# Performance work log

Measured on AMD Instinct MI355X. Metric: run time of the kernel, lower is better.

Reference implementation:

```python
import jax, jax.numpy as jnp
import numpy as np

D_MODEL = 1024
NHEAD = 16
DFF = 4096
EPS = 1e-5


def layer_norm(x, g, b, eps=EPS):
    mu = jnp.mean(x, axis=-1, keepdims=True)
    var = jnp.var(x, axis=-1, keepdims=True)
    return (x - mu) * jax.lax.rsqrt(var + eps) * g + b


def setup_inputs() -> dict:
    key = jax.random.key(0)
    ks = jax.random.split(key, 8)
    S, N, E = 1024, 8, D_MODEL
    s = 0.02
    return {
        "src": jax.random.normal(ks[0], (S, N, E), dtype=jnp.float32),
        "in_proj_w": jax.random.normal(ks[1], (3 * E, E), dtype=jnp.float32) * s,
        "in_proj_b": jnp.zeros((3 * E,), dtype=jnp.float32),
        "out_w": jax.random.normal(ks[2], (E, E), dtype=jnp.float32) * s,
        "out_b": jnp.zeros((E,), dtype=jnp.float32),
        "w1": jax.random.normal(ks[3], (DFF, E), dtype=jnp.float32) * s,
        "b1": jnp.zeros((DFF,), dtype=jnp.float32),
        "w2": jax.random.normal(ks[4], (E, DFF), dtype=jnp.float32) * s,
        "b2": jnp.zeros((E,), dtype=jnp.float32),
        "ln1_g": jnp.ones((E,), dtype=jnp.float32),
        "ln1_b": jnp.zeros((E,), dtype=jnp.float32),
        "ln2_g": jnp.ones((E,), dtype=jnp.float32),
        "ln2_b": jnp.zeros((E,), dtype=jnp.float32),
    }


def reference(src, in_proj_w, in_proj_b, out_w, out_b, w1, b1, w2, b2,
              ln1_g, ln1_b, ln2_g, ln2_b):
    S, N, E = src.shape
    H = NHEAD
    D = E // H
    scale = 1.0 / jnp.sqrt(jnp.asarray(D, src.dtype))

    # fused QKV projection (PyTorch in_proj): [S,N,3E]
    qkv = src @ in_proj_w.T + in_proj_b
    q, k, v = jnp.split(qkv, 3, axis=-1)
    # [S,N,E] -> [N,H,S,D]
    def to_heads(t):
        return t.reshape(S, N, H, D).transpose(1, 2, 0, 3)
    q, k, v = to_heads(q), to_heads(k), to_heads(v)

    # explicit QK^T / softmax / AV (need_weights=True path)
    scores = jnp.einsum('nhsd,nhtd->nhst', q * scale, k)  # [N,H,S,S]
    attn = jax.nn.softmax(scores, axis=-1)
    ctx = jnp.einsum('nhst,nhtd->nhsd', attn, v)          # [N,H,S,D]
    ctx = ctx.transpose(2, 0, 1, 3).reshape(S, N, E)
    attn_out = ctx @ out_w.T + out_b

    # avg over heads (PyTorch default average_attn_weights=True): [N,S,S]
    attn_weights = jnp.mean(attn, axis=1)

    # post-norm residual structure (norm_first=False), dropout=0 (eval)
    x = layer_norm(src + attn_out, ln1_g, ln1_b)
    ff = jax.nn.relu(x @ w1.T + b1) @ w2.T + b2
    x = layer_norm(x + ff, ln2_g, ln2_b)
    return x, attn_weights
```

## Files before the change

kernel.cpp:

```cpp
#include <hip/hip_runtime.h>

typedef __attribute__((ext_vector_type(4))) float f32x4;
typedef __attribute__((ext_vector_type(8))) short short8;
typedef __attribute__((ext_vector_type(4))) unsigned short u16x4;

#define MFMA(a,b,c) __builtin_amdgcn_mfma_f32_16x16x32_bf16(a,b,c,0,0,0)

__device__ __forceinline__ unsigned short f2bf(float x){
    union { float f; unsigned int u; } c; c.f = x;
    unsigned int u = c.u;
    unsigned int r = (u + 0x7fffu + ((u >> 16) & 1u)) >> 16;
    return (unsigned short)r;
}
__device__ __forceinline__ float bf2f(unsigned short h){
    union { unsigned int u; float f; } c; c.u = ((unsigned int)h) << 16;
    return c.f;
}

__device__ __forceinline__ void load16_lds(const unsigned short* g, unsigned short* l){
    __builtin_amdgcn_global_load_lds(
        (const __attribute__((address_space(1))) unsigned int*)g,
        (__attribute__((address_space(3))) unsigned int*)l, 16, 0, 0);
}

#define SWZ_IDX(row, col, stride) \
    ((row)*(stride) + (((((col) >> 3) ^ ((row) & 7)) << 3) | ((col) & 7)))

__global__ __launch_bounds__(256) void cast_f32_bf16(const float* __restrict__ in,
                                                     unsigned short* __restrict__ out, int n4){
    int i = blockIdx.x * 256 + threadIdx.x;
    if (i < n4){
        const float4* in4 = (const float4*)in;
        float4 v = in4[i];
        u16x4 o;
        o[0] = f2bf(v.x); o[1] = f2bf(v.y); o[2] = f2bf(v.z); o[3] = f2bf(v.w);
        ((u16x4*)out)[i] = o;
    }
}

template<int OUT_BF16, int RELU>
__global__ __launch_bounds__(256) void gemm_bt(const unsigned short* __restrict__ A,
                                               const unsigned short* __restrict__ W,
                                               const float* __restrict__ bias,
                                               void* __restrict__ Cout,
                                               int M, int N, int K)
{
    __shared__ unsigned short As[128*32];
    __shared__ unsigned short Bs[128*32];
    const int tid  = threadIdx.x;
    const int wave = tid >> 6, lane = tid & 63;
    const int bm = blockIdx.x, bn = blockIdx.y;
    const int wr = wave >> 1, wc = wave & 1;
    const int lr = lane & 15, lg = lane >> 4;

    f32x4 acc[4][4] = {};

    const size_t arow0 = (size_t)bm * 128;
    const size_t brow0 = (size_t)bn * 128;

    for (int k0 = 0; k0 < K; k0 += 32){
        __syncthreads();
        #pragma unroll
        for (int i = 0; i < 2; ++i){
            int c = i*256 + wave*64 + lane;
            int row = c >> 2, cc = c & 3;
            load16_lds(A + (arow0 + row)*K + k0 + cc*8, As + (size_t)(i*256 + wave*64)*8);
            load16_lds(W + (brow0 + row)*K + k0 + cc*8, Bs + (size_t)(i*256 + wave*64)*8);
        }
        __syncthreads();
        short8 af[4], bfr[4];
        #pragma unroll
        for (int mi = 0; mi < 4; ++mi)
            af[mi] = *(const short8*)(As + (wr*64 + mi*16 + lr)*32 + lg*8);
        #pragma unroll
        for (int ni = 0; ni < 4; ++ni)
            bfr[ni] = *(const short8*)(Bs + (wc*64 + ni*16 + lr)*32 + lg*8);
        #pragma unroll
        for (int mi = 0; mi < 4; ++mi)
            #pragma unroll
            for (int ni = 0; ni < 4; ++ni)
                acc[mi][ni] = MFMA(af[mi], bfr[ni], acc[mi][ni]);
    }

    #pragma unroll
    for (int ni = 0; ni < 4; ++ni){
        int col = bn*128 + wc*64 + ni*16 + lr;
        float bv = bias ? bias[col] : 0.0f;
        #pragma unroll
        for (int mi = 0; mi < 4; ++mi){
            int row0 = bm*128 + wr*64 + mi*16 + lg*4;
            #pragma unroll
            for (int j = 0; j < 4; ++j){
                float v = acc[mi][ni][j] + bv;
                if (RELU) v = v > 0.0f ? v : 0.0f;
                if (OUT_BF16) ((unsigned short*)Cout)[(size_t)(row0+j)*N + col] = f2bf(v);
                else          ((float*)Cout)[(size_t)(row0+j)*N + col] = v;
            }
        }
    }
}

__global__ __launch_bounds__(256) void transpose_v(const unsigned short* __restrict__ qkv,
                                                   unsigned short* __restrict__ vt)
{
    __shared__ unsigned short tile[64][80];
    const int tt = blockIdx.x, h = blockIdx.y, n = blockIdx.z;
    const int tid = threadIdx.x;
    #pragma unroll
    for (int i = 0; i < 2; ++i){
        int c = i*256 + tid;
        int row = c >> 3, cc = c & 7;
        short8 v = *(const short8*)(qkv + ((size_t)(tt*64+row)*8 + n)*3072 + 2048 + h*64 + cc*8);
        *(short8*)&tile[row][cc*8] = v;
    }
    __syncthreads();
    #pragma unroll
    for (int i = 0; i < 2; ++i){
        int c = i*256 + tid;
        int drow = c >> 3, cc = c & 7;
        short8 o;
        #pragma unroll
        for (int j = 0; j < 8; ++j) o[j] = tile[cc*8+j][drow];
        *(short8*)(vt + ((size_t)(n*16+h)*64 + drow)*1024 + tt*64 + cc*8) = o;
    }
}

__global__ __launch_bounds__(256) void attn_fused(const unsigned short* __restrict__ qkv,
                                                  const unsigned short* __restrict__ vt,
                                                  float2* __restrict__ stats,
                                                  unsigned short* __restrict__ ctx)
{
    __shared__ unsigned short qs[32*64];
    __shared__ unsigned short kt[64*64];
    __shared__ unsigned short vtile[64*64];
    __shared__ unsigned short pt[32*64];
    __shared__ float wl[4][32];
    __shared__ float rowinv[32];
    const int qb = blockIdx.x, h = blockIdx.y, n = blockIdx.z;
    const int tid = threadIdx.x;
    const int wave = tid >> 6, lane = tid & 63;
    const int lr = lane & 15, lg = lane >> 4;
    const int s0 = qb * 32;
    const float scale = 0.125f;

    {
        int row = tid >> 3, cc = tid & 7;
        *(short8*)(qs + SWZ_IDX(row, cc*8, 64)) =
            *(const short8*)(qkv + ((size_t)(s0+row)*8 + n)*3072 + h*64 + cc*8);
    }

    float lsum[2][4] = {};
    f32x4 av[2] = {};

    for (int tt = 0; tt < 16; ++tt){
        __syncthreads();
        #pragma unroll
        for (int i = 0; i < 2; ++i){
            int c = i*256 + wave*64 + lane;
            int row = c >> 3, sl = (c & 7) ^ (row & 7);
            load16_lds(qkv + ((size_t)(tt*64+row)*8 + n)*3072 + 1024 + h*64 + sl*8,
                       kt + (size_t)(i*256 + wave*64)*8);
            load16_lds(vt + ((size_t)(n*16+h)*64 + row)*1024 + tt*64 + sl*8,
                       vtile + (size_t)(i*256 + wave*64)*8);
        }
        __syncthreads();

        f32x4 acc[2] = {};
        #pragma unroll
        for (int kk = 0; kk < 2; ++kk){
            short8 b  = *(const short8*)(kt + SWZ_IDX(wave*16 + lr, kk*32 + lg*8, 64));
            short8 a0 = *(const short8*)(qs + SWZ_IDX(lr,          kk*32 + lg*8, 64));
            short8 a1 = *(const short8*)(qs + SWZ_IDX(16 + lr,     kk*32 + lg*8, 64));
            acc[0] = MFMA(a0, b, acc[0]);
            acc[1] = MFMA(a1, b, acc[1]);
        }
        #pragma unroll
        for (int mi = 0; mi < 2; ++mi)
            #pragma unroll
            for (int j = 0; j < 4; ++j){
                float p = __expf(fminf(acc[mi][j] * scale, 80.0f));
                lsum[mi][j] += p;
                pt[SWZ_IDX(mi*16 + lg*4 + j, wave*16 + lr, 64)] = f2bf(p);
            }
        __syncthreads();

        #pragma unroll
        for (int kk = 0; kk < 2; ++kk){
            short8 b  = *(const short8*)(vtile + SWZ_IDX(wave*16 + lr, kk*32 + lg*8, 64));
            short8 a0 = *(const short8*)(pt + SWZ_IDX(lr,      kk*32 + lg*8, 64));
            short8 a1 = *(const short8*)(pt + SWZ_IDX(16 + lr, kk*32 + lg*8, 64));
            av[0] = MFMA(a0, b, av[0]);
            av[1] = MFMA(a1, b, av[1]);
        }
    }

    #pragma unroll
    for (int mi = 0; mi < 2; ++mi)
        #pragma unroll
        for (int j = 0; j < 4; ++j){
            float v = lsum[mi][j];
            v += __shfl_xor(v, 1);
            v += __shfl_xor(v, 2);
            v += __shfl_xor(v, 4);
            v += __shfl_xor(v, 8);
            if (lr == 0) wl[wave][mi*16 + lg*4 + j] = v;
        }
    __syncthreads();
    if (tid < 32){
        float l = wl[0][tid] + wl[1][tid] + wl[2][tid] + wl[3][tid];
        float inv = 1.0f / l;
        rowinv[tid] = inv;
        stats[((size_t)(n*16+h)*1024) + s0 + tid] = make_float2(0.0f, inv * 0.0625f);
    }
    __syncthreads();

    #pragma unroll
    for (int mi = 0; mi < 2; ++mi)
        #pragma unroll
        for (int j = 0; j < 4; ++j){
            int lrow = mi*16 + lg*4 + j;
            int srow = s0 + lrow;
            int d = wave*16 + lr;
            ctx[((size_t)srow*8 + n)*1024 + h*64 + d] = f2bf(av[mi][j] * rowinv[lrow]);
        }
}

__global__ __launch_bounds__(256) void attn_mean(const unsigned short* __restrict__ qkv,
                                                 const float2* __restrict__ stats,
                                                 float* __restrict__ attw)
{
    __shared__ unsigned short qs[16*256];
    __shared__ unsigned short kv[64*256];
    __shared__ float2 smL[16][16];
    const int qb = blockIdx.x, n = blockIdx.y;
    const int tid = threadIdx.x;
    const int wave = tid >> 6, lane = tid & 63;
    const int lr = lane & 15, lg = lane >> 4;
    const int s0 = qb * 16;
    const float scale = 0.125f;

    {
        int head = tid >> 4, row = tid & 15;
        smL[head][row] = stats[((size_t)(n*16+head)*1024) + s0 + row];
    }

    f32x4 racc[16];
    #pragma unroll
    for (int t = 0; t < 16; ++t) racc[t] = (f32x4){0.0f,0.0f,0.0f,0.0f};

    for (int g = 0; g < 4; ++g){
        __syncthreads();
        #pragma unroll
        for (int i = 0; i < 2; ++i){
            int c = i*256 + tid;
            int row = c >> 5, cc = c & 31;
            *(short8*)(qs + SWZ_IDX(row, cc*8, 256)) =
                *(const short8*)(qkv + ((size_t)(s0+row)*8 + n)*3072 + g*256 + cc*8);
        }
        #pragma unroll
        for (int tt = 0; tt < 16; ++tt){
            __syncthreads();
            #pragma unroll
            for (int i = 0; i < 8; ++i){
                int c = i*256 + wave*64 + lane;
                int row = c >> 5, sd = c & 31;
                int sl = sd ^ (row & 7);
                load16_lds(qkv + ((size_t)(tt*64+row)*8 + n)*3072 + 1024 + g*256 + sl*8,
                           kv + (size_t)(i*256 + wave*64)*8);
            }
            __syncthreads();
            #pragma unroll
            for (int hh = 0; hh < 4; ++hh){
                f32x4 acc = {0.0f,0.0f,0.0f,0.0f};
                #pragma unroll
                for (int kk = 0; kk < 2; ++kk){
                    short8 b = *(const short8*)(kv + SWZ_IDX(wave*16 + lr, hh*64 + kk*32 + lg*8, 256));
                    short8 a = *(const short8*)(qs + SWZ_IDX(lr,           hh*64 + kk*32 + lg*8, 256));
                    acc = MFMA(a, b, acc);
                }
                #pragma unroll
                for (int j = 0; j < 4; ++j){
                    float2 mc = smL[g*4 + hh][lg*4 + j];
                    racc[tt][j] += __expf(fminf(acc[j]*scale, 80.0f) - mc.x) * mc.y;
                }
            }
        }
    }
    float* base = attw + (size_t)n*1024*1024;
    #pragma unroll
    for (int tt = 0; tt < 16; ++tt)
        #pragma unroll
        for (int j = 0; j < 4; ++j)
            base[(size_t)(s0 + lg*4 + j)*1024 + tt*64 + wave*16 + lr] = racc[tt][j];
}

__global__ __launch_bounds__(256) void add_ln(const float* __restrict__ a,
                                              const float* __restrict__ b,
                                              const float* __restrict__ g,
                                              const float* __restrict__ be,
                                              float* __restrict__ out32,
                                              unsigned short* __restrict__ outbf)
{
    __shared__ float red[8];
    const int row = blockIdx.x;
    const int tid = threadIdx.x;
    const int wave = tid >> 6, lane = tid & 63;
    float4 va = ((const float4*)(a + (size_t)row*1024))[tid];
    float4 vb = ((const float4*)(b + (size_t)row*1024))[tid];
    float x0 = va.x + vb.x, x1 = va.y + vb.y, x2 = va.z + vb.z, x3 = va.w + vb.w;
    float s  = x0 + x1 + x2 + x3;
    float sq = x0*x0 + x1*x1 + x2*x2 + x3*x3;
    #pragma unroll
    for (int off = 1; off < 64; off <<= 1){
        s  += __shfl_xor(s,  off);
        sq += __shfl_xor(sq, off);
    }
    if (lane == 0){ red[wave] = s; red[4+wave] = sq; }
    __syncthreads();
    s  = red[0] + red[1] + red[2] + red[3];
    sq = red[4] + red[5] + red[6] + red[7];
    float mean = s * (1.0f/1024.0f);
    float var  = sq * (1.0f/1024.0f) - mean*mean;
    float rstd = rsqrtf(var + 1e-5f);
    int c = tid * 4;
    float4 vg = ((const float4*)(g  + c))[0];
    float4 vbeta = ((const float4*)(be + c))[0];
    float y0 = (x0-mean)*rstd*vg.x + vbeta.x;
    float y1 = (x1-mean)*rstd*vg.y + vbeta.y;
    float y2 = (x2-mean)*rstd*vg.z + vbeta.z;
    float y3 = (x3-mean)*rstd*vg.w + vbeta.w;
    float4 o; o.x=y0; o.y=y1; o.z=y2; o.w=y3;
    ((float4*)(out32 + (size_t)row*1024))[tid] = o;
    if (outbf){
        u16x4 ob; ob[0]=f2bf(y0); ob[1]=f2bf(y1); ob[2]=f2bf(y2); ob[3]=f2bf(y3);
        ((u16x4*)(outbf + (size_t)row*1024))[tid] = ob;
    }
}

extern "C" void kernel_launch(void* const* d_in, const int* in_sizes, int n_in,
                              void* d_out, int out_size, void* d_ws, size_t ws_size,
                              hipStream_t stream)
{
    (void)in_sizes; (void)n_in; (void)out_size; (void)ws_size;
    const float* src  = (const float*)d_in[0];
    const float* wqkv = (const float*)d_in[1];
    const float* bqkv = (const float*)d_in[2];
    const float* wout = (const float*)d_in[3];
    const float* bout = (const float*)d_in[4];
    const float* w1   = (const float*)d_in[5];
    const float* b1   = (const float*)d_in[6];
    const float* w2   = (const float*)d_in[7];
    const float* b2   = (const float*)d_in[8];
    const float* g1   = (const float*)d_in[9];
    const float* be1  = (const float*)d_in[10];
    const float* g2   = (const float*)d_in[11];
    const float* be2  = (const float*)d_in[12];

    char* ws = (char*)d_ws;
    const size_t MB = 1ull << 20;
    unsigned short* wqkv_bf = (unsigned short*)(ws + 0*MB);
    unsigned short* wout_bf = (unsigned short*)(ws + 6*MB);
    unsigned short* w1_bf   = (unsigned short*)(ws + 8*MB);
    unsigned short* w2_bf   = (unsigned short*)(ws + 16*MB);
    unsigned short* src_bf  = (unsigned short*)(ws + 24*MB);
    unsigned short* x1_bf   = (unsigned short*)(ws + 24*MB);
    unsigned short* qkv_bf  = (unsigned short*)(ws + 40*MB);
    unsigned short* vt_bf   = (unsigned short*)(ws + 88*MB);
    unsigned short* ff1_bf  = (unsigned short*)(ws + 40*MB);
    unsigned short* ctx_bf  = (unsigned short*)(ws + 104*MB);
    float* attn_out = (float*)(ws + 120*MB);
    float* ff2_f32  = (float*)(ws + 120*MB);
    float* x1_f32   = (float*)(ws + 152*MB);
    float2* stats   = (float2*)(ws + 184*MB);

    float* x_out    = (float*)d_out;
    float* attw_out = (float*)d_out + (size_t)8192*1024;

    auto cast = [&](const float* in, unsigned short* out, int nelem){
        int n4 = nelem / 4;
        hipLaunchKernelGGL(cast_f32_bf16, dim3((n4 + 255)/256), dim3(256), 0, stream, in, out, n4);
    };
    cast(wqkv, wqkv_bf, 3072*1024);
    cast(wout, wout_bf, 1024*1024);
    cast(w1,   w1_bf,   4096*1024);
    cast(w2,   w2_bf,   1024*4096);
    cast(src,  src_bf,  8192*1024);

    hipLaunchKernelGGL((gemm_bt<1,0>), dim3(64,24), dim3(256), 0, stream,
                       src_bf, wqkv_bf, bqkv, (void*)qkv_bf, 8192, 3072, 1024);
    hipLaunchKernelGGL(transpose_v, dim3(16,16,8), dim3(256), 0, stream, qkv_bf, vt_bf);
    hipLaunchKernelGGL(attn_fused, dim3(32,16,8), dim3(256), 0, stream,
                       qkv_bf, vt_bf, stats, ctx_bf);
    hipLaunchKernelGGL(attn_mean, dim3(64,8), dim3(256), 0, stream,
                       qkv_bf, stats, attw_out);
    hipLaunchKernelGGL((gemm_bt<0,0>), dim3(64,8), dim3(256), 0, stream,
                       ctx_bf, wout_bf, bout, (void*)attn_out, 8192, 1024, 1024);
    hipLaunchKernelGGL(add_ln, dim3(8192), dim3(256), 0, stream,
                       src, attn_out, g1, be1, x1_f32, x1_bf);
    hipLaunchKernelGGL((gemm_bt<1,1>), dim3(64,32), dim3(256), 0, stream,
                       x1_bf, w1_bf, b1, (void*)ff1_bf, 8192, 4096, 1024);
    hipLaunchKernelGGL((gemm_bt<0,0>), dim3(64,8), dim3(256), 0, stream,
                       ff1_bf, w2_bf, b2, (void*)ff2_f32, 8192, 1024, 4096);
    hipLaunchKernelGGL(add_ln, dim3(8192), dim3(256), 0, stream,
                       x1_f32, ff2_f32, g2, be2, x_out, nullptr);
}
```

Before: 619.3 us.

## Double-buffer per-wave K tiles in attn_mean and drop block barriers

Restructures the head-averaged attention weight kernel. The full Q row block for all heads is loaded once, the loop order becomes key-tile outer and head-pair inner, and each wave streams its own 16 key rows into a double-buffered LDS slot with vmcnt waits in place of block-wide __syncthreads. The accumulator shrinks from 16 f32x4 to one, and results are written after each key tile. This is meant to overlap K loads with MFMA/exp work, remove barrier stalls and cut register pressure, at the cost of larger LDS use and hand-tuned waitcnt ordering.

Result: faster. 578.9 us (-6.5%).

```diff
diff --git a/kernel.cpp b/kernel.cpp
--- a/kernel.cpp
+++ b/kernel.cpp
@@ -229,8 +229,8 @@
                                                  const float2* __restrict__ stats,
                                                  float* __restrict__ attw)
 {
-    __shared__ unsigned short qs[16*256];
-    __shared__ unsigned short kv[64*256];
+    __shared__ unsigned short qs[16*1024];
+    __shared__ unsigned short kv[2][4][16*128];
     __shared__ float2 smL[16][16];
     const int qb = blockIdx.x, n = blockIdx.y;
     const int tid = threadIdx.x;
@@ -243,55 +243,63 @@
         int head = tid >> 4, row = tid & 15;
         smL[head][row] = stats[((size_t)(n*16+head)*1024) + s0 + row];
     }
-
-    f32x4 racc[16];
-    #pragma unroll
-    for (int t = 0; t < 16; ++t) racc[t] = (f32x4){0.0f,0.0f,0.0f,0.0f};
-
-    for (int g = 0; g < 4; ++g){
-        __syncthreads();
-        #pragma unroll
-        for (int i = 0; i < 2; ++i){
-            int c = i*256 + tid;
-            int row = c >> 5, cc = c & 31;
-            *(short8*)(qs + SWZ_IDX(row, cc*8, 256)) =
-                *(const short8*)(qkv + ((size_t)(s0+row)*8 + n)*3072 + g*256 + cc*8);
-        }
-        #pragma unroll
-        for (int tt = 0; tt < 16; ++tt){
-            __syncthreads();
+    #pragma unroll
+    for (int i = 0; i < 8; ++i){
+        int c = i*256 + tid;
+        int row = c >> 7, cc = c & 127;
+        *(short8*)(qs + SWZ_IDX(row, cc*8, 1024)) =
+            *(const short8*)(qkv + ((size_t)(s0+row)*8 + n)*3072 + cc*8);
+    }
+
+    unsigned short* kvw = &kv[0][wave][0];
+    const int KVBUF = 4*16*128;
+
+    auto stage = [&](int buf, int tt, int g){
+        #pragma unroll
+        for (int i = 0; i < 4; ++i){
+            int c2 = i*64 + lane;
+            int rw = c2 >> 4;
+            int sd = c2 & 15;
+            int sl = sd ^ (rw & 7);
+            int trow = tt*64 + wave*16 + rw;
+            load16_lds(qkv + ((size_t)trow*8 + n)*3072 + 1024 + g*128 + sl*8,
+                       kvw + buf*KVBUF + i*512);
+        }
+    };
+
+    __syncthreads();
+    stage(0, 0, 0);
+
+    float* obase = attw + (size_t)n*1024*1024;
+    int r = 0;
+    for (int tt = 0; tt < 16; ++tt){
+        f32x4 racc = {0.0f, 0.0f, 0.0f, 0.0f};
+        for (int g = 0; g < 8; ++g, ++r){
+            int nr = r + 1;
+            if (nr < 128) stage(nr & 1, nr >> 3, nr & 7);
+            if (r < 127) asm volatile("s_waitcnt vmcnt(4)" ::: "memory");
+            else         asm volatile("s_waitcnt vmcnt(0)" ::: "memory");
+            const unsigned short* kb = kvw + (r & 1)*KVBUF;
             #pragma unroll
-            for (int i = 0; i < 8; ++i){
-                int c = i*256 + wave*64 + lane;
-                int row = c >> 5, sd = c & 31;
-                int sl = sd ^ (row & 7);
-                load16_lds(qkv + ((size_t)(tt*64+row)*8 + n)*3072 + 1024 + g*256 + sl*8,
-                           kv + (size_t)(i*256 + wave*64)*8);
-            }
-            __syncthreads();
-            #pragma unroll
-            for (int hh = 0; hh < 4; ++hh){
-                f32x4 acc = {0.0f,0.0f,0.0f,0.0f};
+            for (int hh = 0; hh < 2; ++hh){
+                f32x4 acc = {0.0f, 0.0f, 0.0f, 0.0f};
                 #pragma unroll
                 for (int kk = 0; kk < 2; ++kk){
-                    short8 b = *(const short8*)(kv + SWZ_IDX(wave*16 + lr, hh*64 + kk*32 + lg*8, 256));
-                    short8 a = *(const short8*)(qs + SWZ_IDX(lr,           hh*64 + kk*32 + lg*8, 256));
+                    short8 b = *(const short8*)(kb + SWZ_IDX(lr, hh*64 + kk*32 + lg*8, 128));
+                    short8 a = *(const short8*)(qs + SWZ_IDX(lr, g*128 + hh*64 + kk*32 + lg*8, 1024));
                     acc = MFMA(a, b, acc);
                 }
                 #pragma unroll
                 for (int j = 0; j < 4; ++j){
-                    float2 mc = smL[g*4 + hh][lg*4 + j];
-                    racc[tt][j] += __expf(fminf(acc[j]*scale, 80.0f) - mc.x) * mc.y;
+                    float2 mc = smL[g*2 + hh][lg*4 + j];
+                    racc[j] += __expf(fminf(acc[j]*scale, 80.0f) - mc.x) * mc.y;
                 }
             }
         }
-    }
-    float* base = attw + (size_t)n*1024*1024;
-    #pragma unroll
-    for (int tt = 0; tt < 16; ++tt)
         #pragma unroll
         for (int j = 0; j < 4; ++j)
-            base[(size_t)(s0 + lg*4 + j)*1024 + tt*64 + wave*16 + lr] = racc[tt][j];
+            obase[(size_t)(s0 + lg*4 + j)*1024 + tt*64 + wave*16 + lr] = racc[j];
+    }
 }
 
 __global__ __launch_bounds__(256) void add_ln(const float* __restrict__ a,
```
